# Performance work log

Measured on AMD Instinct MI355X. Metric: run time of the kernel, lower is better.

The kernel has to match this reference:

```python
import jax, jax.numpy as jnp
import numpy as np

H_HEADS = 8
HIDDEN = 512
D_K = HIDDEN // H_HEADS


def setup_inputs() -> dict:
    key = jax.random.key(0)
    ks = jax.random.split(key, 16)
    B, T = 4, 1024
    P = 2 * T - 1
    s = 0.02
    inp = {
        "x": jax.random.normal(ks[0], (B, T, HIDDEN), dtype=jnp.float32),
        "pos_emb": jax.random.normal(ks[1], (1, P, HIDDEN), dtype=jnp.float32),
        "Wq": jax.random.normal(ks[2], (HIDDEN, HIDDEN), dtype=jnp.float32) * s,
        "bq": jnp.zeros((HIDDEN,), dtype=jnp.float32),
        "Wk": jax.random.normal(ks[3], (HIDDEN, HIDDEN), dtype=jnp.float32) * s,
        "bk": jnp.zeros((HIDDEN,), dtype=jnp.float32),
        "Wv": jax.random.normal(ks[4], (HIDDEN, HIDDEN), dtype=jnp.float32) * s,
        "bv": jnp.zeros((HIDDEN,), dtype=jnp.float32),
        "Wp": jax.random.normal(ks[5], (HIDDEN, HIDDEN), dtype=jnp.float32) * s,
        "bp": jnp.zeros((HIDDEN,), dtype=jnp.float32),
        "Wo": jax.random.normal(ks[6], (HIDDEN, HIDDEN), dtype=jnp.float32) * s,
        "bo": jnp.zeros((HIDDEN,), dtype=jnp.float32),
        "pos_bias_u": jax.random.normal(ks[7], (H_HEADS, D_K), dtype=jnp.float32) * s,
        "pos_bias_v": jax.random.normal(ks[8], (H_HEADS, D_K), dtype=jnp.float32) * s,
    }
    return inp


def rel_shift(x):
    # x: (B, H, T, P). Transformer-XL relative shift.
    B, H, T, P = x.shape
    x = jnp.pad(x, ((0, 0), (0, 0), (0, 0), (1, 0)))  # (B,H,T,P+1)
    x = x.reshape(B, H, P + 1, T)[:, :, 1:, :]          # drop first row
    return x.reshape(B, H, T, P)


def reference(x, pos_emb, Wq, bq, Wk, bk, Wv, bv, Wp, bp, Wo, bo, pos_bias_u, pos_bias_v):
    B, T, _ = x.shape
    Hh, d = H_HEADS, D_K
    scale = 1.0 / jnp.sqrt(jnp.asarray(d, dtype=x.dtype))

    q = (x @ Wq + bq).reshape(B, T, Hh, d)                       # (B,T,H,d)
    k = (x @ Wk + bk).reshape(B, T, Hh, d).transpose(0, 2, 1, 3)  # (B,H,T,d)
    v = (x @ Wv + bv).reshape(B, T, Hh, d).transpose(0, 2, 1, 3)  # (B,H,T,d)
    P = pos_emb.shape[1]
    p = (pos_emb @ Wp + bp).reshape(pos_emb.shape[0], P, Hh, d).transpose(0, 2, 1, 3)  # (1,H,P,d)

    q_u = (q + pos_bias_u).transpose(0, 2, 1, 3)  # (B,H,T,d)
    q_v = (q + pos_bias_v).transpose(0, 2, 1, 3)  # (B,H,T,d)

    # content-position term with rel-shift (broadcast over batch dim of p)
    matrix_bd = jnp.matmul(q_v, p.transpose(0, 1, 3, 2))  # (B,H,T,P)
    matrix_bd = rel_shift(matrix_bd)[:, :, :, :T] * scale  # (B,H,T,T)

    # content-content term + additive bias, scaled softmax
    scores = jnp.matmul(q_u, k.transpose(0, 1, 3, 2)) * scale + matrix_bd
    attn = jax.nn.softmax(scores.astype(jnp.float32), axis=-1).astype(x.dtype)
    out = jnp.matmul(attn, v)                 # (B,H,T,d)
    out = out.transpose(0, 2, 1, 3).reshape(B, T, Hh * d)
    return out @ Wo + bo
```

## Files before the change

kernel.cpp:

```cpp
#include <hip/hip_runtime.h>
#include <math.h>

#define BATCH 4
#define SEQ   1024
#define HID   512
#define NHEAD 8

typedef unsigned short u16;
typedef unsigned int   u32;
typedef short  short8 __attribute__((ext_vector_type(8)));
typedef float  f32x4  __attribute__((ext_vector_type(4)));

__device__ __forceinline__ u16 f2bf(float x) {
  u32 u = __builtin_bit_cast(u32, x);
  u32 r = (u + 0x7FFFu + ((u >> 16) & 1u)) >> 16;
  return (u16)r;
}

__global__ __launch_bounds__(256)
void cvt_two(const float* __restrict__ x, const float* __restrict__ pe,
             u16* __restrict__ xb, u16* __restrict__ peb) {
  int i = blockIdx.x * 256 + threadIdx.x;
  const float* s;
  u16* d;
  if (i < 524288) {
    s = x; d = xb;
  } else {
    i -= 524288;
    if (i >= 262016) return;
    s = pe; d = peb;
  }
  float4 v = *(const float4*)&s[(size_t)i * 4];
  ushort4 o;
  o.x = f2bf(v.x); o.y = f2bf(v.y); o.z = f2bf(v.z); o.w = f2bf(v.w);
  *(ushort4*)&d[(size_t)i * 4] = o;
}

__global__ __launch_bounds__(256)
void transpose_w(const float* w0, const float* w1, const float* w2,
                 const float* w3, const float* w4, u16* __restrict__ wt) {
  const float* src;
  switch (blockIdx.z) {
    case 0: src = w0; break;
    case 1: src = w1; break;
    case 2: src = w2; break;
    case 3: src = w3; break;
    default: src = w4; break;
  }
  u16* dst = wt + (size_t)blockIdx.z * 512 * 512;
  __shared__ float t[32][33];
  const int tx = threadIdx.x, ty = threadIdx.y;
  const int k0 = blockIdx.x * 32, n0 = blockIdx.y * 32;
#pragma unroll
  for (int r = 0; r < 4; ++r)
    t[ty + 8 * r][tx] = src[(size_t)(k0 + ty + 8 * r) * 512 + n0 + tx];
  __syncthreads();
#pragma unroll
  for (int r = 0; r < 4; ++r)
    dst[(size_t)(n0 + ty + 8 * r) * 512 + k0 + tx] = f2bf(t[tx][ty + 8 * r]);
}

template <int MF, int NF>
__device__ __forceinline__ void gemm_core(const u16* __restrict__ A,
                                          const u16* __restrict__ Bt,
                                          int m0, int n0, u16* As, u16* Bs,
                                          f32x4 (&acc)[MF][NF]) {
  const int tid = threadIdx.x;
  const int wid = tid >> 6, lane = tid & 63;
  const int lr = lane & 15, lg = lane >> 4;
  const int wm = wid >> 1, wn = wid & 1;
  const int srow = tid >> 3, sc = tid & 7;
#pragma unroll
  for (int i = 0; i < MF; ++i)
#pragma unroll
    for (int j = 0; j < NF; ++j) acc[i][j] = (f32x4)0.f;

  for (int kt = 0; kt < 8; ++kt) {
    const int k0 = kt * 64;
    short8 la[MF], lb[NF];
#pragma unroll
    for (int r = 0; r < MF; ++r)
      la[r] = *(const short8*)&A[(size_t)(m0 + srow + 32 * r) * 512 + k0 + sc * 8];
#pragma unroll
    for (int r = 0; r < NF; ++r)
      lb[r] = *(const short8*)&Bt[(size_t)(n0 + srow + 32 * r) * 512 + k0 + sc * 8];
    __syncthreads();
#pragma unroll
    for (int r = 0; r < MF; ++r) {
      int row = srow + 32 * r;
      *(short8*)&As[row * 64 + ((sc ^ (row & 7)) * 8)] = la[r];
    }
#pragma unroll
    for (int r = 0; r < NF; ++r) {
      int row = srow + 32 * r;
      *(short8*)&Bs[row * 64 + ((sc ^ (row & 7)) * 8)] = lb[r];
    }
    __syncthreads();
#pragma unroll
    for (int kc = 0; kc < 2; ++kc) {
      const int ch = kc * 4 + lg;
      short8 af[MF], bfr[NF];
#pragma unroll
      for (int mt = 0; mt < MF; ++mt) {
        int row = wm * (MF * 16) + mt * 16 + lr;
        af[mt] = *(const short8*)&As[row * 64 + ((ch ^ (row & 7)) * 8)];
      }
#pragma unroll
      for (int nt = 0; nt < NF; ++nt) {
        int row = wn * (NF * 16) + nt * 16 + lr;
        bfr[nt] = *(const short8*)&Bs[row * 64 + ((ch ^ (row & 7)) * 8)];
      }
#pragma unroll
      for (int mt = 0; mt < MF; ++mt)
#pragma unroll
        for (int nt = 0; nt < NF; ++nt)
          acc[mt][nt] = __builtin_amdgcn_mfma_f32_16x16x32_bf16(
              af[mt], bfr[nt], acc[mt][nt], 0, 0, 0);
    }
  }
}

__global__ __launch_bounds__(256)
void gemm_qkvp(const u16* __restrict__ xbf, const u16* __restrict__ pebf,
               const u16* __restrict__ wt,
               const float* __restrict__ bq, const float* __restrict__ bk,
               const float* __restrict__ bv, const float* __restrict__ bp,
               const float* __restrict__ pbu, const float* __restrict__ pbv,
               u16* __restrict__ qu, u16* __restrict__ qv,
               u16* __restrict__ kk, u16* __restrict__ vt,
               u16* __restrict__ pp) {
  __shared__ __align__(16) u16 As[128 * 64];
  __shared__ __align__(16) u16 Bs[128 * 64];
  const int z = blockIdx.z;
  if (z == 3 && blockIdx.y >= 16) return;
  const u16* A = (z == 3) ? pebf : xbf;
  const u16* Bt = wt + (size_t)z * 512 * 512;
  const float* bias = (z == 0) ? bq : (z == 1) ? bk : (z == 2) ? bv : bp;
  const int m0 = blockIdx.y * 128, n0 = blockIdx.x * 128;

  f32x4 acc[4][4];
  gemm_core<4, 4>(A, Bt, m0, n0, As, Bs, acc);

  const int tid = threadIdx.x, wid = tid >> 6, lane = tid & 63;
  const int lr = lane & 15, lg = lane >> 4, wm = wid >> 1, wn = wid & 1;
#pragma unroll
  for (int mt = 0; mt < 4; ++mt)
#pragma unroll
    for (int nt = 0; nt < 4; ++nt) {
      const int col = n0 + wn * 64 + nt * 16 + lr;
      const int rb = m0 + wm * 64 + mt * 16 + lg * 4;
      const float bcol = bias[col];
      if (z == 0) {
        const float uu = pbu[col], vv = pbv[col];
#pragma unroll
        for (int q = 0; q < 4; ++q) {
          float val = acc[mt][nt][q] + bcol;
          qu[(size_t)(rb + q) * 512 + col] = f2bf(val + uu);
          qv[(size_t)(rb + q) * 512 + col] = f2bf(val + vv);
        }
      } else if (z == 1) {
#pragma unroll
        for (int q = 0; q < 4; ++q)
          kk[(size_t)(rb + q) * 512 + col] = f2bf(acc[mt][nt][q] + bcol);
      } else if (z == 2) {
        ushort4 pk;
        pk.x = f2bf(acc[mt][nt][0] + bcol);
        pk.y = f2bf(acc[mt][nt][1] + bcol);
        pk.z = f2bf(acc[mt][nt][2] + bcol);
        pk.w = f2bf(acc[mt][nt][3] + bcol);
        int bb = rb >> 10, tl = rb & 1023;
        *(ushort4*)&vt[(size_t)((bb * 8 + (col >> 6)) * 64 + (col & 63)) * 1024 + tl] = pk;
      } else {
#pragma unroll
        for (int q = 0; q < 4; ++q)
          if (rb + q < 2047)
            pp[(size_t)(rb + q) * 512 + col] = f2bf(acc[mt][nt][q] + bcol);
      }
    }
}

__global__ __launch_bounds__(256)
void gemm_wo(const u16* __restrict__ ao, const u16* __restrict__ wt,
             const float* __restrict__ bo, float* __restrict__ out) {
  __shared__ __align__(16) u16 As[64 * 64];
  __shared__ __align__(16) u16 Bs[64 * 64];
  const int m0 = blockIdx.y * 64, n0 = blockIdx.x * 64;
  f32x4 acc[2][2];
  gemm_core<2, 2>(ao, wt + (size_t)4 * 512 * 512, m0, n0, As, Bs, acc);
  const int tid = threadIdx.x, wid = tid >> 6, lane = tid & 63;
  const int lr = lane & 15, lg = lane >> 4, wm = wid >> 1, wn = wid & 1;
#pragma unroll
  for (int mt = 0; mt < 2; ++mt)
#pragma unroll
    for (int nt = 0; nt < 2; ++nt) {
      const int col = n0 + wn * 32 + nt * 16 + lr;
      const int rb = m0 + wm * 32 + mt * 16 + lg * 4;
      const float bcol = bo[col];
#pragma unroll
      for (int q = 0; q < 4; ++q)
        out[(size_t)(rb + q) * 512 + col] = acc[mt][nt][q] + bcol;
    }
}

__global__ __launch_bounds__(512)
void attn_mfma(const u16* __restrict__ quP, const u16* __restrict__ qvP,
               const u16* __restrict__ kP, const u16* __restrict__ vtP,
               const u16* __restrict__ pP, u16* __restrict__ ao) {
  __shared__ __align__(16) u16 SM[56832];
  u16* Ps = SM + 16384;

  const int tid = threadIdx.x;
  const int wid = tid >> 6, lane = tid & 63;
  const int lr = lane & 15, lg = lane >> 4;
  const int grp = wid >> 2, wq = wid & 3;
  const int t0 = blockIdx.x * 128, h = blockIdx.y, b = blockIdx.z;
  const int base0 = 896 - t0;

  u16* Ksg = SM + grp * 4096;
  u16* Vsg = SM + 8192 + grp * 4096;
  float* wbf = (float*)(SM + 32768) + wid * 1504;
  u16* esw = (u16*)wbf;

  short8 aqu[2][2], aqv[2][2];
#pragma unroll
  for (int f = 0; f < 2; ++f)
#pragma unroll
    for (int kc = 0; kc < 2; ++kc) {
      size_t g = (size_t)(b * SEQ + t0 + 32 * wq + 16 * f + lr) * 512 + h * 64 +
                 kc * 32 + lg * 8;
      aqu[f][kc] = *(const short8*)&quP[g];
      aqv[f][kc] = *(const short8*)&qvP[g];
    }
  short8 ones;
#pragma unroll
  for (int i = 0; i < 8; ++i) ones[i] = (short)0x3F80;

  float mrun[2] = {-1e30f, -1e30f};
  f32x4 cL[2], cO[2][4];
#pragma unroll
  for (int f = 0; f < 2; ++f) {
    cL[f] = (f32x4)0.f;
#pragma unroll
    for (int nt = 0; nt < 4; ++nt) cO[f][nt] = (f32x4)0.f;
  }

#pragma unroll
  for (int r = 0; r < 2; ++r) {
    int idx = tid + 512 * r;
    int row = idx >> 3, sc = idx & 7;
    short8 lk = *(const short8*)&kP[(size_t)(b * SEQ + row) * 512 + h * 64 + sc * 8];
    short8 lv = *(const short8*)&vtP[(size_t)((b * 8 + h) * 64 + (row & 63)) * 1024 +
                                     (row >> 6) * 64 + sc * 8];
    *(short8*)&SM[(row >> 6) * 4096 + (row & 63) * 64 + ((sc ^ (row & 7)) * 8)] = lk;
    *(short8*)&SM[8192 + (row >> 6) * 4096 + (row & 63) * 64 + ((sc ^ (row & 7)) * 8)] = lv;
  }
#pragma unroll
  for (int r = 0; r < 4; ++r) {
    int idx = tid + 512 * r;
    int prow = idx >> 3, sc = idx & 7;
    short8 lp = *(const short8*)&pP[(size_t)(base0 + prow) * 512 + h * 64 + sc * 8];
    *(short8*)&Ps[prow * 64 + ((sc ^ (prow & 7)) * 8)] = lp;
  }
  __syncthreads();

  for (int s = 0; s < 8; ++s) {
    short8 nk[2], nv[2], np[2];
    if (s < 7) {
      const int jn = 128 * (s + 1);
#pragma unroll
      for (int r = 0; r < 2; ++r) {
        int idx = tid + 512 * r;
        int row = idx >> 3, sc = idx & 7;
        nk[r] = *(const short8*)&kP[(size_t)(b * SEQ + jn + row) * 512 + h * 64 + sc * 8];
        nv[r] = *(const short8*)&vtP[(size_t)((b * 8 + h) * 64 + (row & 63)) * 1024 +
                                     jn + (row >> 6) * 64 + sc * 8];
        np[r] = *(const short8*)&pP[(size_t)(base0 + 256 + 128 * s + row) * 512 +
                                    h * 64 + sc * 8];
      }
    }

    f32x4 cKT[2][4];
#pragma unroll
    for (int f = 0; f < 2; ++f)
#pragma unroll
      for (int nt = 0; nt < 4; ++nt) cKT[f][nt] = (f32x4)0.f;
    __builtin_amdgcn_s_setprio(1);
#pragma unroll
    for (int kc = 0; kc < 2; ++kc) {
      const int ch = kc * 4 + lg;
#pragma unroll
      for (int nt = 0; nt < 4; ++nt) {
        int krow = nt * 16 + lr;
        short8 bk = *(const short8*)&Ksg[krow * 64 + ((ch ^ (krow & 7)) * 8)];
        cKT[0][nt] = __builtin_amdgcn_mfma_f32_16x16x32_bf16(bk, aqu[0][kc], cKT[0][nt], 0, 0, 0);
        cKT[1][nt] = __builtin_amdgcn_mfma_f32_16x16x32_bf16(bk, aqu[1][kc], cKT[1][nt], 0, 0, 0);
      }
    }
    __builtin_amdgcn_s_setprio(0);

    short8 bvr[2][4];
#pragma unroll
    for (int kc = 0; kc < 2; ++kc) {
      const int ch = kc * 4 + lg;
#pragma unroll
      for (int nt = 0; nt < 4; ++nt) {
        int vr = nt * 16 + lr;
        bvr[kc][nt] = *(const short8*)&Vsg[vr * 64 + ((ch ^ (vr & 7)) * 8)];
      }
    }

#pragma unroll
    for (int f = 0; f < 2; ++f) {
      const int poff = 112 - 32 * wq - 16 * f + 64 * grp + 128 * s;
      f32x4 cPT[5];
#pragma unroll
      for (int i = 0; i < 5; ++i) cPT[i] = (f32x4)0.f;
      __builtin_amdgcn_s_setprio(1);
#pragma unroll
      for (int kc = 0; kc < 2; ++kc) {
        const int ch = kc * 4 + lg;
        const int swz = (ch ^ (lr & 7)) * 8;
#pragma unroll
        for (int pt = 0; pt < 5; ++pt) {
          int pos = (poff + pt * 16 + lr) & 255;
          short8 bp = *(const short8*)&Ps[pos * 64 + swz];
          cPT[pt] = __builtin_amdgcn_mfma_f32_16x16x32_bf16(bp, aqv[f][kc], cPT[pt], 0, 0, 0);
        }
      }
      __builtin_amdgcn_s_setprio(0);

#pragma unroll
      for (int pt = 0; pt < 5; ++pt)
        *(f32x4*)&wbf[lr * 84 + pt * 16 + lg * 4] = cPT[pt];
      float sv[4][4];
#pragma unroll
      for (int nt = 0; nt < 4; ++nt)
#pragma unroll
        for (int q = 0; q < 4; ++q)
          sv[nt][q] = 0.125f * (cKT[f][nt][q] +
                                wbf[lr * 84 + 16 * nt + lg * 4 + q + 15 - lr]);

      float tm = sv[0][0];
#pragma unroll
      for (int nt = 0; nt < 4; ++nt)
#pragma unroll
        for (int q = 0; q < 4; ++q) tm = fmaxf(tm, sv[nt][q]);
      tm = fmaxf(tm, __shfl_xor(tm, 16));
      tm = fmaxf(tm, __shfl_xor(tm, 32));
      if (__any(tm > mrun[f] + 8.f)) {
        float mnew = fmaxf(mrun[f], tm);
        float corr = __expf(mrun[f] - mnew);
        mrun[f] = mnew;
        float cc[4];
#pragma unroll
        for (int q = 0; q < 4; ++q)
          cc[q] = __shfl(corr, (lane & 48) | (lg * 4 + q));
#pragma unroll
        for (int q = 0; q < 4; ++q) {
          cL[f][q] *= cc[q];
#pragma unroll
          for (int nt = 0; nt < 4; ++nt) cO[f][nt][q] *= cc[q];
        }
      }

#pragma unroll
      for (int nt = 0; nt < 4; ++nt) {
        float e0 = __expf(sv[nt][0] - mrun[f]);
        float e1 = __expf(sv[nt][1] - mrun[f]);
        float e2 = __expf(sv[nt][2] - mrun[f]);
        float e3 = __expf(sv[nt][3] - mrun[f]);
        uint2 pk;
        pk.x = (u32)f2bf(e0) | ((u32)f2bf(e1) << 16);
        pk.y = (u32)f2bf(e2) | ((u32)f2bf(e3) << 16);
        int g = 2 * nt + (lg >> 1);
        *(uint2*)&esw[lr * 64 + ((g ^ (lr & 7)) * 8) + (lg & 1) * 4] = pk;
      }

      __builtin_amdgcn_s_setprio(1);
#pragma unroll
      for (int kc = 0; kc < 2; ++kc) {
        const int ch = kc * 4 + lg;
        short8 pa = *(const short8*)&esw[lr * 64 + ((ch ^ (lr & 7)) * 8)];
        cL[f] = __builtin_amdgcn_mfma_f32_16x16x32_bf16(pa, ones, cL[f], 0, 0, 0);
#pragma unroll
        for (int nt = 0; nt < 4; ++nt)
          cO[f][nt] = __builtin_amdgcn_mfma_f32_16x16x32_bf16(pa, bvr[kc][nt], cO[f][nt], 0, 0, 0);
      }
      __builtin_amdgcn_s_setprio(0);
    }

    __syncthreads();
    if (s < 7) {
#pragma unroll
      for (int r = 0; r < 2; ++r) {
        int idx = tid + 512 * r;
        int row = idx >> 3, sc = idx & 7;
        *(short8*)&SM[(row >> 6) * 4096 + (row & 63) * 64 + ((sc ^ (row & 7)) * 8)] = nk[r];
        *(short8*)&SM[8192 + (row >> 6) * 4096 + (row & 63) * 64 + ((sc ^ (row & 7)) * 8)] = nv[r];
        int pos = (128 * s + row) & 255;
        *(short8*)&Ps[pos * 64 + ((sc ^ (pos & 7)) * 8)] = np[r];
      }
    }
    __syncthreads();
  }

  float m_c[2][4];
#pragma unroll
  for (int f = 0; f < 2; ++f)
#pragma unroll
    for (int q = 0; q < 4; ++q)
      m_c[f][q] = __shfl(mrun[f], (lane & 48) | (lg * 4 + q));

  float* ob = (float*)SM;
  float* mlb = (float*)(SM + 16384);
  if (grp == 1) {
#pragma unroll
    for (int f = 0; f < 2; ++f) {
#pragma unroll
      for (int nt = 0; nt < 4; ++nt)
#pragma unroll
        for (int q = 0; q < 4; ++q)
          ob[(wq * 32 + 16 * f + 4 * lg + q) * 64 + nt * 16 + lr] = cO[f][nt][q];
      if (lr == 0) {
#pragma unroll
        for (int q = 0; q < 4; ++q) {
          int rr = wq * 32 + 16 * f + 4 * lg + q;
          mlb[rr * 2 + 0] = m_c[f][q];
          mlb[rr * 2 + 1] = cL[f][q];
        }
      }
    }
  }
  __syncthreads();
  if (grp == 0) {
#pragma unroll
    for (int f = 0; f < 2; ++f) {
      float ws0[4], ws1[4];
#pragma unroll
      for (int q = 0; q < 4; ++q) {
        int rr = wq * 32 + 16 * f + 4 * lg + q;
        float m1 = mlb[rr * 2 + 0], l1 = mlb[rr * 2 + 1];
        float M = fmaxf(m_c[f][q], m1);
        float w0 = __expf(m_c[f][q] - M), w1 = __expf(m1 - M);
        float inv = 1.f / (w0 * cL[f][q] + w1 * l1);
        ws0[q] = w0 * inv;
        ws1[q] = w1 * inv;
      }
#pragma unroll
      for (int nt = 0; nt < 4; ++nt)
#pragma unroll
        for (int q = 0; q < 4; ++q) {
          int rr = wq * 32 + 16 * f + 4 * lg + q;
          float o1 = ob[rr * 64 + nt * 16 + lr];
          float val = ws0[q] * cO[f][nt][q] + ws1[q] * o1;
          ao[(size_t)(b * SEQ + t0 + rr) * 512 + h * 64 + nt * 16 + lr] = f2bf(val);
        }
    }
  }
}

extern "C" void kernel_launch(void* const* d_in, const int* in_sizes, int n_in,
                              void* d_out, int out_size, void* d_ws, size_t ws_size,
                              hipStream_t stream) {
  const float* x   = (const float*)d_in[0];
  const float* pe  = (const float*)d_in[1];
  const float* Wq  = (const float*)d_in[2];
  const float* bq  = (const float*)d_in[3];
  const float* Wk  = (const float*)d_in[4];
  const float* bk  = (const float*)d_in[5];
  const float* Wv  = (const float*)d_in[6];
  const float* bv  = (const float*)d_in[7];
  const float* Wp  = (const float*)d_in[8];
  const float* bp  = (const float*)d_in[9];
  const float* Wo  = (const float*)d_in[10];
  const float* bo  = (const float*)d_in[11];
  const float* pbu = (const float*)d_in[12];
  const float* pbv = (const float*)d_in[13];

  char* ws = (char*)d_ws;
  size_t o = 0;
  auto alloc = [&](size_t bytes) { size_t r = o; o += (bytes + 255) & ~(size_t)255; return r; };
  u16* x_bf  = (u16*)(ws + alloc((size_t)4096 * 512 * 2));
  u16* pe_bf = (u16*)(ws + alloc((size_t)2048 * 512 * 2));
  u16* wt    = (u16*)(ws + alloc((size_t)5 * 512 * 512 * 2));
  u16* qu    = (u16*)(ws + alloc((size_t)4096 * 512 * 2));
  u16* qv    = (u16*)(ws + alloc((size_t)4096 * 512 * 2));
  u16* kk    = (u16*)(ws + alloc((size_t)4096 * 512 * 2));
  u16* vt    = (u16*)(ws + alloc((size_t)4096 * 512 * 2));
  u16* pp    = (u16*)(ws + alloc((size_t)2048 * 512 * 2));
  u16* ao    = (u16*)(ws + alloc((size_t)4096 * 512 * 2));

  dim3 blk(256);
  cvt_two<<<dim3(3072), blk, 0, stream>>>(x, pe, x_bf, pe_bf);
  transpose_w<<<dim3(16, 16, 5), dim3(32, 8), 0, stream>>>(Wq, Wk, Wv, Wp, Wo, wt);
  hipMemsetAsync(pp + (size_t)2047 * 512, 0, 512 * 2, stream);

  gemm_qkvp<<<dim3(4, 32, 4), blk, 0, stream>>>(x_bf, pe_bf, wt, bq, bk, bv, bp,
                                                pbu, pbv, qu, qv, kk, vt, pp);
  attn_mfma<<<dim3(8, NHEAD, BATCH), dim3(512), 0, stream>>>(qu, qv, kk, vt, pp, ao);
  gemm_wo<<<dim3(8, 64), blk, 0, stream>>>(ao, wt, bo, (float*)d_out);
}
```

Before: 76.82 us.

## Fuse fp32-to-bf16 input conversion into QKVP GEMM and reuse P fragments in attention

Removes the separate cvt_two kernel and the memset by loading fp32 x and pos_emb directly in the QKVP GEMM tile loader and converting them to bf16 in registers. Out-of-range rows are clamped instead of being read from a zero-padded buffer. In the attention kernel, the positional LDS fragments loaded for the first query half are cached in registers and reused for the second half, shifted by one 16-row tile, which cuts LDS reads. The trade-off is twice the global read bytes for the A operand inside the GEMM, plus extra registers in the attention kernel. The pp row 2047 is no longer zeroed, so correctness depends on that row never being read or not affecting results.

```diff
diff --git a/kernel.cpp b/kernel.cpp
--- a/kernel.cpp
+++ b/kernel.cpp
@@ -15,25 +15,6 @@
   u32 u = __builtin_bit_cast(u32, x);
   u32 r = (u + 0x7FFFu + ((u >> 16) & 1u)) >> 16;
   return (u16)r;
-}
-
-__global__ __launch_bounds__(256)
-void cvt_two(const float* __restrict__ x, const float* __restrict__ pe,
-             u16* __restrict__ xb, u16* __restrict__ peb) {
-  int i = blockIdx.x * 256 + threadIdx.x;
-  const float* s;
-  u16* d;
-  if (i < 524288) {
-    s = x; d = xb;
-  } else {
-    i -= 524288;
-    if (i >= 262016) return;
-    s = pe; d = peb;
-  }
-  float4 v = *(const float4*)&s[(size_t)i * 4];
-  ushort4 o;
-  o.x = f2bf(v.x); o.y = f2bf(v.y); o.z = f2bf(v.z); o.w = f2bf(v.w);
-  *(ushort4*)&d[(size_t)i * 4] = o;
 }
 
 __global__ __launch_bounds__(256)
@@ -60,10 +41,10 @@
     dst[(size_t)(n0 + ty + 8 * r) * 512 + k0 + tx] = f2bf(t[tx][ty + 8 * r]);
 }
 
-template <int MF, int NF>
-__device__ __forceinline__ void gemm_core(const u16* __restrict__ A,
+template <int MF, int NF, bool AF32>
+__device__ __forceinline__ void gemm_core(const void* __restrict__ Ap,
                                           const u16* __restrict__ Bt,
-                                          int m0, int n0, u16* As, u16* Bs,
+                                          int m0, int n0, int M, u16* As, u16* Bs,
                                           f32x4 (&acc)[MF][NF]) {
   const int tid = threadIdx.x;
   const int wid = tid >> 6, lane = tid & 63;
@@ -79,8 +60,21 @@
     const int k0 = kt * 64;
     short8 la[MF], lb[NF];
 #pragma unroll
-    for (int r = 0; r < MF; ++r)
-      la[r] = *(const short8*)&A[(size_t)(m0 + srow + 32 * r) * 512 + k0 + sc * 8];
+    for (int r = 0; r < MF; ++r) {
+      int row = m0 + srow + 32 * r;
+      if (row > M - 1) row = M - 1;
+      if (AF32) {
+        const float* A32 = (const float*)Ap;
+        float4 a0 = *(const float4*)&A32[(size_t)row * 512 + k0 + sc * 8];
+        float4 a1 = *(const float4*)&A32[(size_t)row * 512 + k0 + sc * 8 + 4];
+        la[r][0] = (short)f2bf(a0.x); la[r][1] = (short)f2bf(a0.y);
+        la[r][2] = (short)f2bf(a0.z); la[r][3] = (short)f2bf(a0.w);
+        la[r][4] = (short)f2bf(a1.x); la[r][5] = (short)f2bf(a1.y);
+        la[r][6] = (short)f2bf(a1.z); la[r][7] = (short)f2bf(a1.w);
+      } else {
+        la[r] = *(const short8*)&((const u16*)Ap)[(size_t)row * 512 + k0 + sc * 8];
+      }
+    }
 #pragma unroll
     for (int r = 0; r < NF; ++r)
       lb[r] = *(const short8*)&Bt[(size_t)(n0 + srow + 32 * r) * 512 + k0 + sc * 8];
@@ -121,7 +115,7 @@
 }
 
 __global__ __launch_bounds__(256)
-void gemm_qkvp(const u16* __restrict__ xbf, const u16* __restrict__ pebf,
+void gemm_qkvp(const float* __restrict__ x, const float* __restrict__ pe,
                const u16* __restrict__ wt,
                const float* __restrict__ bq, const float* __restrict__ bk,
                const float* __restrict__ bv, const float* __restrict__ bp,
@@ -133,13 +127,14 @@
   __shared__ __align__(16) u16 Bs[128 * 64];
   const int z = blockIdx.z;
   if (z == 3 && blockIdx.y >= 16) return;
-  const u16* A = (z == 3) ? pebf : xbf;
+  const void* A = (z == 3) ? (const void*)pe : (const void*)x;
+  const int M = (z == 3) ? 2047 : 4096;
   const u16* Bt = wt + (size_t)z * 512 * 512;
   const float* bias = (z == 0) ? bq : (z == 1) ? bk : (z == 2) ? bv : bp;
   const int m0 = blockIdx.y * 128, n0 = blockIdx.x * 128;
 
   f32x4 acc[4][4];
-  gemm_core<4, 4>(A, Bt, m0, n0, As, Bs, acc);
+  gemm_core<4, 4, true>(A, Bt, m0, n0, M, As, Bs, acc);
 
   const int tid = threadIdx.x, wid = tid >> 6, lane = tid & 63;
   const int lr = lane & 15, lg = lane >> 4, wm = wid >> 1, wn = wid & 1;
@@ -186,7 +181,7 @@
   __shared__ __align__(16) u16 Bs[64 * 64];
   const int m0 = blockIdx.y * 64, n0 = blockIdx.x * 64;
   f32x4 acc[2][2];
-  gemm_core<2, 2>(ao, wt + (size_t)4 * 512 * 512, m0, n0, As, Bs, acc);
+  gemm_core<2, 2, false>(ao, wt + (size_t)4 * 512 * 512, m0, n0, 4096, As, Bs, acc);
   const int tid = threadIdx.x, wid = tid >> 6, lane = tid & 63;
   const int lr = lane & 15, lg = lane >> 4, wm = wid >> 1, wn = wid & 1;
 #pragma unroll
@@ -309,6 +304,7 @@
       }
     }
 
+    short8 bpc[2][4];
 #pragma unroll
     for (int f = 0; f < 2; ++f) {
       const int poff = 112 - 32 * wq - 16 * f + 64 * grp + 128 * s;
@@ -320,11 +316,21 @@
       for (int kc = 0; kc < 2; ++kc) {
         const int ch = kc * 4 + lg;
         const int swz = (ch ^ (lr & 7)) * 8;
-#pragma unroll
-        for (int pt = 0; pt < 5; ++pt) {
-          int pos = (poff + pt * 16 + lr) & 255;
-          short8 bp = *(const short8*)&Ps[pos * 64 + swz];
-          cPT[pt] = __builtin_amdgcn_mfma_f32_16x16x32_bf16(bp, aqv[f][kc], cPT[pt], 0, 0, 0);
+        if (f == 0) {
+#pragma unroll
+          for (int pt = 0; pt < 5; ++pt) {
+            int pos = (poff + pt * 16 + lr) & 255;
+            short8 bp = *(const short8*)&Ps[pos * 64 + swz];
+            if (pt < 4) bpc[kc][pt] = bp;
+            cPT[pt] = __builtin_amdgcn_mfma_f32_16x16x32_bf16(bp, aqv[0][kc], cPT[pt], 0, 0, 0);
+          }
+        } else {
+          int pos = (poff + lr) & 255;
+          short8 bp0 = *(const short8*)&Ps[pos * 64 + swz];
+          cPT[0] = __builtin_amdgcn_mfma_f32_16x16x32_bf16(bp0, aqv[1][kc], cPT[0], 0, 0, 0);
+#pragma unroll
+          for (int pt = 1; pt < 5; ++pt)
+            cPT[pt] = __builtin_amdgcn_mfma_f32_16x16x32_bf16(bpc[kc][pt - 1], aqv[1][kc], cPT[pt], 0, 0, 0);
         }
       }
       __builtin_amdgcn_s_setprio(0);
@@ -480,22 +486,17 @@
   char* ws = (char*)d_ws;
   size_t o = 0;
   auto alloc = [&](size_t bytes) { size_t r = o; o += (bytes + 255) & ~(size_t)255; return r; };
-  u16* x_bf  = (u16*)(ws + alloc((size_t)4096 * 512 * 2));
-  u16* pe_bf = (u16*)(ws + alloc((size_t)2048 * 512 * 2));
-  u16* wt    = (u16*)(ws + alloc((size_t)5 * 512 * 512 * 2));
-  u16* qu    = (u16*)(ws + alloc((size_t)4096 * 512 * 2));
-  u16* qv    = (u16*)(ws + alloc((size_t)4096 * 512 * 2));
-  u16* kk    = (u16*)(ws + alloc((size_t)4096 * 512 * 2));
-  u16* vt    = (u16*)(ws + alloc((size_t)4096 * 512 * 2));
-  u16* pp    = (u16*)(ws + alloc((size_t)2048 * 512 * 2));
-  u16* ao    = (u16*)(ws + alloc((size_t)4096 * 512 * 2));
+  u16* wt = (u16*)(ws + alloc((size_t)5 * 512 * 512 * 2));
+  u16* qu = (u16*)(ws + alloc((size_t)4096 * 512 * 2));
+  u16* qv = (u16*)(ws + alloc((size_t)4096 * 512 * 2));
+  u16* kk = (u16*)(ws + alloc((size_t)4096 * 512 * 2));
+  u16* vt = (u16*)(ws + alloc((size_t)4096 * 512 * 2));
+  u16* pp = (u16*)(ws + alloc((size_t)2048 * 512 * 2));
+  u16* ao = (u16*)(ws + alloc((size_t)4096 * 512 * 2));
 
   dim3 blk(256);
-  cvt_two<<<dim3(3072), blk, 0, stream>>>(x, pe, x_bf, pe_bf);
   transpose_w<<<dim3(16, 16, 5), dim3(32, 8), 0, stream>>>(Wq, Wk, Wv, Wp, Wo, wt);
-  hipMemsetAsync(pp + (size_t)2047 * 512, 0, 512 * 2, stream);
-
-  gemm_qkvp<<<dim3(4, 32, 4), blk, 0, stream>>>(x_bf, pe_bf, wt, bq, bk, bv, bp,
+  gemm_qkvp<<<dim3(4, 32, 4), blk, 0, stream>>>(x, pe, wt, bq, bk, bv, bp,
                                                 pbu, pbv, qu, qv, kk, vt, pp);
   attn_mfma<<<dim3(8, NHEAD, BATCH), dim3(512), 0, stream>>>(qu, qv, kk, vt, pp, ao);
   gemm_wo<<<dim3(8, 64), blk, 0, stream>>>(ao, wt, bo, (float*)d_out);
```

Result: slower. 79.20 us (+3.1%).

## Prefetch next GEMM K-tile into registers and reuse P fragments in attention

Applied to the files above, without the earlier changes.

The GEMM core now loads the next 64-wide K slice into a second set of registers while the current tile is consumed from LDS, overlapping global loads with MFMA work. The A-row index is clamped so the pos_emb GEMM does not read past its last valid row, which allows removing the separate memset launch for the padding row of p. In the attention kernel, the second query fragment reuses four of the five P-position fragments already loaded for the first, cutting LDS reads. Extra live registers may reduce occupancy, and the padding row of p is no longer zeroed.

```diff
diff --git a/kernel.cpp b/kernel.cpp
--- a/kernel.cpp
+++ b/kernel.cpp
@@ -63,7 +63,7 @@
 template <int MF, int NF>
 __device__ __forceinline__ void gemm_core(const u16* __restrict__ A,
                                           const u16* __restrict__ Bt,
-                                          int m0, int n0, u16* As, u16* Bs,
+                                          int m0, int n0, int M, u16* As, u16* Bs,
                                           f32x4 (&acc)[MF][NF]) {
   const int tid = threadIdx.x;
   const int wid = tid >> 6, lane = tid & 63;
@@ -75,15 +75,18 @@
 #pragma unroll
     for (int j = 0; j < NF; ++j) acc[i][j] = (f32x4)0.f;
 
+  short8 la[MF], lb[NF], la2[MF], lb2[NF];
+#pragma unroll
+  for (int r = 0; r < MF; ++r) {
+    int row = m0 + srow + 32 * r;
+    row = row > M - 1 ? M - 1 : row;
+    la[r] = *(const short8*)&A[(size_t)row * 512 + sc * 8];
+  }
+#pragma unroll
+  for (int r = 0; r < NF; ++r)
+    lb[r] = *(const short8*)&Bt[(size_t)(n0 + srow + 32 * r) * 512 + sc * 8];
+
   for (int kt = 0; kt < 8; ++kt) {
-    const int k0 = kt * 64;
-    short8 la[MF], lb[NF];
-#pragma unroll
-    for (int r = 0; r < MF; ++r)
-      la[r] = *(const short8*)&A[(size_t)(m0 + srow + 32 * r) * 512 + k0 + sc * 8];
-#pragma unroll
-    for (int r = 0; r < NF; ++r)
-      lb[r] = *(const short8*)&Bt[(size_t)(n0 + srow + 32 * r) * 512 + k0 + sc * 8];
     __syncthreads();
 #pragma unroll
     for (int r = 0; r < MF; ++r) {
@@ -95,6 +98,18 @@
       int row = srow + 32 * r;
       *(short8*)&Bs[row * 64 + ((sc ^ (row & 7)) * 8)] = lb[r];
     }
+    if (kt < 7) {
+      const int k1 = (kt + 1) * 64;
+#pragma unroll
+      for (int r = 0; r < MF; ++r) {
+        int row = m0 + srow + 32 * r;
+        row = row > M - 1 ? M - 1 : row;
+        la2[r] = *(const short8*)&A[(size_t)row * 512 + k1 + sc * 8];
+      }
+#pragma unroll
+      for (int r = 0; r < NF; ++r)
+        lb2[r] = *(const short8*)&Bt[(size_t)(n0 + srow + 32 * r) * 512 + k1 + sc * 8];
+    }
     __syncthreads();
 #pragma unroll
     for (int kc = 0; kc < 2; ++kc) {
@@ -117,6 +132,10 @@
           acc[mt][nt] = __builtin_amdgcn_mfma_f32_16x16x32_bf16(
               af[mt], bfr[nt], acc[mt][nt], 0, 0, 0);
     }
+#pragma unroll
+    for (int r = 0; r < MF; ++r) la[r] = la2[r];
+#pragma unroll
+    for (int r = 0; r < NF; ++r) lb[r] = lb2[r];
   }
 }
 
@@ -134,12 +153,13 @@
   const int z = blockIdx.z;
   if (z == 3 && blockIdx.y >= 16) return;
   const u16* A = (z == 3) ? pebf : xbf;
+  const int M = (z == 3) ? 2047 : 4096;
   const u16* Bt = wt + (size_t)z * 512 * 512;
   const float* bias = (z == 0) ? bq : (z == 1) ? bk : (z == 2) ? bv : bp;
   const int m0 = blockIdx.y * 128, n0 = blockIdx.x * 128;
 
   f32x4 acc[4][4];
-  gemm_core<4, 4>(A, Bt, m0, n0, As, Bs, acc);
+  gemm_core<4, 4>(A, Bt, m0, n0, M, As, Bs, acc);
 
   const int tid = threadIdx.x, wid = tid >> 6, lane = tid & 63;
   const int lr = lane & 15, lg = lane >> 4, wm = wid >> 1, wn = wid & 1;
@@ -186,7 +206,7 @@
   __shared__ __align__(16) u16 Bs[64 * 64];
   const int m0 = blockIdx.y * 64, n0 = blockIdx.x * 64;
   f32x4 acc[2][2];
-  gemm_core<2, 2>(ao, wt + (size_t)4 * 512 * 512, m0, n0, As, Bs, acc);
+  gemm_core<2, 2>(ao, wt + (size_t)4 * 512 * 512, m0, n0, 4096, As, Bs, acc);
   const int tid = threadIdx.x, wid = tid >> 6, lane = tid & 63;
   const int lr = lane & 15, lg = lane >> 4, wm = wid >> 1, wn = wid & 1;
 #pragma unroll
@@ -309,6 +329,7 @@
       }
     }
 
+    short8 bpc[2][4];
 #pragma unroll
     for (int f = 0; f < 2; ++f) {
       const int poff = 112 - 32 * wq - 16 * f + 64 * grp + 128 * s;
@@ -320,11 +341,21 @@
       for (int kc = 0; kc < 2; ++kc) {
         const int ch = kc * 4 + lg;
         const int swz = (ch ^ (lr & 7)) * 8;
-#pragma unroll
-        for (int pt = 0; pt < 5; ++pt) {
-          int pos = (poff + pt * 16 + lr) & 255;
-          short8 bp = *(const short8*)&Ps[pos * 64 + swz];
-          cPT[pt] = __builtin_amdgcn_mfma_f32_16x16x32_bf16(bp, aqv[f][kc], cPT[pt], 0, 0, 0);
+        if (f == 0) {
+#pragma unroll
+          for (int pt = 0; pt < 5; ++pt) {
+            int pos = (poff + pt * 16 + lr) & 255;
+            short8 bp = *(const short8*)&Ps[pos * 64 + swz];
+            if (pt < 4) bpc[kc][pt] = bp;
+            cPT[pt] = __builtin_amdgcn_mfma_f32_16x16x32_bf16(bp, aqv[0][kc], cPT[pt], 0, 0, 0);
+          }
+        } else {
+          int pos = (poff + lr) & 255;
+          short8 bp0 = *(const short8*)&Ps[pos * 64 + swz];
+          cPT[0] = __builtin_amdgcn_mfma_f32_16x16x32_bf16(bp0, aqv[1][kc], cPT[0], 0, 0, 0);
+#pragma unroll
+          for (int pt = 1; pt < 5; ++pt)
+            cPT[pt] = __builtin_amdgcn_mfma_f32_16x16x32_bf16(bpc[kc][pt - 1], aqv[1][kc], cPT[pt], 0, 0, 0);
         }
       }
       __builtin_amdgcn_s_setprio(0);
@@ -493,8 +524,6 @@
   dim3 blk(256);
   cvt_two<<<dim3(3072), blk, 0, stream>>>(x, pe, x_bf, pe_bf);
   transpose_w<<<dim3(16, 16, 5), dim3(32, 8), 0, stream>>>(Wq, Wk, Wv, Wp, Wo, wt);
-  hipMemsetAsync(pp + (size_t)2047 * 512, 0, 512 * 2, stream);
-
   gemm_qkvp<<<dim3(4, 32, 4), blk, 0, stream>>>(x_bf, pe_bf, wt, bq, bk, bv, bp,
                                                 pbu, pbv, qu, qv, kk, vt, pp);
   attn_mfma<<<dim3(8, NHEAD, BATCH), dim3(512), 0, stream>>>(qu, qv, kk, vt, pp, ao);
```

Result: slower. 79.23 us (+3.1%).
